# Kernel optimization log

Hardware: AMD Instinct MI355X
Metric: run time of the kernel (lower is better)

The kernel has to match this reference:

```python
import jax, jax.numpy as jnp
import numpy as np

B, S, D = 2, 2048, 2048
H, KVH, HD = 16, 4, 128
GROUPS = H // KVH
SCALE = HD ** -0.5


def rotate_half(x):
    half = x.shape[-1] // 2
    return jnp.concatenate((-x[..., half:], x[..., :half]), axis=-1)


def apply_rope(q, k, cos, sin):
    # q,k: [B,S,H,HD]; cos,sin: [S,HD//2] -> repeat_interleave(2) -> [S,HD]
    cos = jnp.repeat(cos, 2, axis=-1)[None, :, None, :]
    sin = jnp.repeat(sin, 2, axis=-1)[None, :, None, :]
    return q * cos + rotate_half(q) * sin, k * cos + rotate_half(k) * sin


def setup_inputs() -> dict:
    key = jax.random.key(0)
    ks = jax.random.split(key, 8)
    inp = {
        'x': jax.random.normal(ks[0], (B, S, D), dtype=jnp.float32),
        'cos': jnp.cos(jnp.arange(S, dtype=jnp.float32)[:, None] * (1.0 / (10000.0 ** (jnp.arange(HD // 2, dtype=jnp.float32) / (HD // 2))))[None, :].reshape(1, HD // 2)),
        'sin': None,
        'mask': jnp.tril(jnp.ones((S, S), dtype=bool))[None, None, :, :],
        'Wq': jax.random.normal(ks[1], (D, H * HD), dtype=jnp.float32) * (D ** -0.5),
        'Wk': jax.random.normal(ks[2], (D, KVH * HD), dtype=jnp.float32) * (D ** -0.5),
        'Wv': jax.random.normal(ks[3], (D, KVH * HD), dtype=jnp.float32) * (D ** -0.5),
        'Wo': jax.random.normal(ks[4], (H * HD, D), dtype=jnp.float32) * ((H * HD) ** -0.5),
    }
    inv_freq = 1.0 / (10000.0 ** (jnp.arange(0, HD // 2, dtype=jnp.float32) / (HD // 2)))
    freqs = jnp.arange(S, dtype=jnp.float32)[:, None] * inv_freq[None, :]  # [S, HD//2]
    inp['cos'] = jnp.cos(freqs)
    inp['sin'] = jnp.sin(freqs)
    return inp


def reference(x, cos, sin, mask, Wq, Wk, Wv, Wo):
    b, s, _ = x.shape
    q = (x @ Wq).reshape(b, s, H, HD)    # [B,S,H,HD]
    k = (x @ Wk).reshape(b, s, KVH, HD)  # [B,S,KVH,HD]
    v = (x @ Wv).reshape(b, s, KVH, HD)
    q, k = apply_rope(q, k, cos, sin)
    q = q.transpose(0, 2, 1, 3)  # [B,H,S,HD]
    k = k.transpose(0, 2, 1, 3)  # [B,KVH,S,HD]
    v = v.transpose(0, 2, 1, 3)
    k = jnp.repeat(k, GROUPS, axis=1)  # [B,H,S,HD]
    v = jnp.repeat(v, GROUPS, axis=1)
    scores = jnp.einsum('bhqd,bhkd->bhqk', q, k) * SCALE
    scores = jnp.where(mask, scores, -jnp.inf)
    attn = jax.nn.softmax(scores, axis=-1)
    out = jnp.einsum('bhqk,bhkd->bhqd', attn, v)
    out = out.transpose(0, 2, 1, 3).reshape(b, s, H * HD)
    return out @ Wo
```

## Files before the change

### kernel.cpp

```cpp
#include <hip/hip_runtime.h>
#include <hip/hip_bf16.h>
#include <cstdint>
#include <type_traits>

typedef __attribute__((ext_vector_type(8))) short short8;
typedef __attribute__((ext_vector_type(4))) float floatx4;

constexpr int S_LEN = 2048;
constexpr float ATTN_SCALE = 0.08838834764831845f;
constexpr float LOG2E = 1.4426950408889634f;
constexpr float CP = ATTN_SCALE * LOG2E;

__device__ __forceinline__ void gl_lds16(const void* gp, void* lp) {
  __builtin_amdgcn_global_load_lds(
      (__attribute__((address_space(1))) void*)(uintptr_t)gp,
      (__attribute__((address_space(3))) void*)lp,
      16, 0, 0);
}

__device__ __forceinline__ float rowmax16(float x) {
  union { float f; int i; } a, b;
  a.f = x;
  b.i = __builtin_amdgcn_update_dpp(0, a.i, 0x121, 0xF, 0xF, true);
  x = fmaxf(x, b.f); a.f = x;
  b.i = __builtin_amdgcn_update_dpp(0, a.i, 0x122, 0xF, 0xF, true);
  x = fmaxf(x, b.f); a.f = x;
  b.i = __builtin_amdgcn_update_dpp(0, a.i, 0x124, 0xF, 0xF, true);
  x = fmaxf(x, b.f); a.f = x;
  b.i = __builtin_amdgcn_update_dpp(0, a.i, 0x128, 0xF, 0xF, true);
  return fmaxf(x, b.f);
}

__device__ __forceinline__ void rope8(short8 x0, short8 x1, const float* ca,
                                      const float* sa, const float* cb,
                                      const float* sb, short8& y0, short8& y1) {
#pragma unroll
  for (int e = 0; e < 8; ++e) {
    union { short s; __hip_bfloat16 h; } u0, u1, w0, w1;
    u0.s = x0[e]; u1.s = x1[e];
    float f0 = __bfloat162float(u0.h), f1 = __bfloat162float(u1.h);
    int j = e >> 1;
    w0.h = __float2bfloat16(f0 * ca[j] - f1 * sa[j]);
    w1.h = __float2bfloat16(f1 * cb[j] + f0 * sb[j]);
    y0[e] = w0.s; y1[e] = w1.s;
  }
}

__device__ __forceinline__ void tr32(const float* __restrict__ src,
                                     __hip_bfloat16* __restrict__ dst,
                                     int blk, int nblk_x, int N, int tid,
                                     float (*tile)[33]) {
  int n0 = (blk % nblk_x) * 32, k0 = (blk / nblk_x) * 32;
  int tx = tid & 31, ty = tid >> 5;
#pragma unroll
  for (int i = ty; i < 32; i += 8)
    tile[i][tx] = src[(size_t)(k0 + i) * N + n0 + tx];
  __syncthreads();
#pragma unroll
  for (int i = ty; i < 32; i += 8)
    dst[(size_t)(n0 + i) * 2048 + k0 + tx] = __float2bfloat16(tile[tx][i]);
}

__global__ void prep_kernel(const float* __restrict__ x,
                            const float* __restrict__ Wq,
                            const float* __restrict__ Wk,
                            const float* __restrict__ Wv,
                            const float* __restrict__ Wo,
                            __hip_bfloat16* __restrict__ xb,
                            __hip_bfloat16* __restrict__ wqkvt,
                            __hip_bfloat16* __restrict__ wot) {
  __shared__ float tile[32][33];
  int bx = blockIdx.x, tid = threadIdx.x;
  if (bx < 8192) {
    int i = bx * 256 + tid;
    float4 f = reinterpret_cast<const float4*>(x)[i];
    union { unsigned long long u64; __hip_bfloat16 h[4]; } u;
    u.h[0] = __float2bfloat16(f.x);
    u.h[1] = __float2bfloat16(f.y);
    u.h[2] = __float2bfloat16(f.z);
    u.h[3] = __float2bfloat16(f.w);
    reinterpret_cast<unsigned long long*>(xb)[i] = u.u64;
  } else if (bx < 12288) {
    tr32(Wq, wqkvt, bx - 8192, 64, 2048, tid, tile);
  } else if (bx < 13312) {
    tr32(Wk, wqkvt + 2048 * 2048, bx - 12288, 16, 512, tid, tile);
  } else if (bx < 14336) {
    tr32(Wv, wqkvt + 2560 * 2048, bx - 13312, 16, 512, tid, tile);
  } else {
    tr32(Wo, wot, bx - 14336, 64, 2048, tid, tile);
  }
}

__global__ __launch_bounds__(256, 2) void qkv_gemm_kernel(
    const __hip_bfloat16* __restrict__ A,
    const __hip_bfloat16* __restrict__ Bt,
    __hip_bfloat16* __restrict__ qbuf,
    __hip_bfloat16* __restrict__ kbuf,
    __hip_bfloat16* __restrict__ vbuf,
    const float* __restrict__ cosb,
    const float* __restrict__ sinb) {
  constexpr int K = 2048;
  __shared__ __align__(16) __hip_bfloat16 lds[2 * 128 * 64];
  const int tid = threadIdx.x;
  const int wave = tid >> 6, lane = tid & 63;
  const int quad = lane >> 4, l15 = lane & 15;
  const int wm = wave >> 1, wn = wave & 1;
  const int m0 = blockIdx.y * 128, n0 = blockIdx.x * 128;

  floatx4 acc[4][4] = {};
  const __hip_bfloat16* Ab = A + (size_t)m0 * K;
  const __hip_bfloat16* Bb = Bt + (size_t)n0 * K;
  const int i0 = wave * 4;

  for (int k0 = 0; k0 < K; k0 += 64) {
#pragma unroll
    for (int j = 0; j < 4; ++j) {
      const int i = i0 + j;
      const int kchunk = i >> 1;
      const int row = ((i & 1) << 6) | lane;
      gl_lds16(Ab + (size_t)row * K + (k0 + kchunk * 8), &lds[i * 512]);
      gl_lds16(Bb + (size_t)row * K + (k0 + kchunk * 8), &lds[8192 + i * 512]);
    }
    __syncthreads();
#pragma unroll
    for (int kk = 0; kk < 2; ++kk) {
      short8 a[4], b[4];
#pragma unroll
      for (int mi = 0; mi < 4; ++mi)
        a[mi] = *(const short8*)&lds[((((kk << 2) | quad) * 128) + wm * 64 + mi * 16 + l15) * 8];
#pragma unroll
      for (int ni = 0; ni < 4; ++ni)
        b[ni] = *(const short8*)&lds[8192 + ((((kk << 2) | quad) * 128) + wn * 64 + ni * 16 + l15) * 8];
#pragma unroll
      for (int mi = 0; mi < 4; ++mi)
#pragma unroll
        for (int ni = 0; ni < 4; ++ni)
          acc[mi][ni] = __builtin_amdgcn_mfma_f32_16x16x32_bf16(a[mi], b[ni], acc[mi][ni], 0, 0, 0);
    }
    __syncthreads();
  }

  const bool isv = (n0 >= 2560);
  short* lds2 = (short*)lds;
#pragma unroll
  for (int mi = 0; mi < 4; ++mi)
#pragma unroll
    for (int ni = 0; ni < 4; ++ni)
#pragma unroll
      for (int r = 0; r < 4; ++r) {
        int row = wm * 64 + mi * 16 + quad * 4 + r;
        int col = wn * 64 + ni * 16 + l15;
        union { short s; __hip_bfloat16 h; } u;
        u.h = __float2bfloat16(acc[mi][ni][r]);
        if (isv) lds2[col * 128 + row] = u.s;
        else     lds2[row * 128 + col] = u.s;
      }
  __syncthreads();

  const int c8 = tid & 7, d0 = c8 * 8;
  if (n0 < 2048) {
#pragma unroll
    for (int j = 0; j < 4; ++j) {
      int rr = (tid >> 3) + 32 * j;
      int rowg = m0 + rr;
      int s = rowg & (S_LEN - 1);
      float ca[4], sa[4], cb[4], sb[4];
      *(float4*)ca = *(const float4*)&cosb[s * 64 + c8 * 4];
      *(float4*)sa = *(const float4*)&sinb[s * 64 + c8 * 4];
      *(float4*)cb = *(const float4*)&cosb[s * 64 + 32 + c8 * 4];
      *(float4*)sb = *(const float4*)&sinb[s * 64 + 32 + c8 * 4];
      short8 x0 = *(const short8*)&lds2[rr * 128 + d0];
      short8 x1 = *(const short8*)&lds2[rr * 128 + 64 + d0];
      short8 y0, y1;
      rope8(x0, x1, ca, sa, cb, sb, y0, y1);
      *(short8*)(qbuf + (size_t)rowg * 2048 + n0 + d0) = y0;
      *(short8*)(qbuf + (size_t)rowg * 2048 + n0 + 64 + d0) = y1;
    }
  } else if (!isv) {
    const int kvh = (n0 - 2048) >> 7;
#pragma unroll
    for (int j = 0; j < 4; ++j) {
      int rr = (tid >> 3) + 32 * j;
      int rowg = m0 + rr;
      int s = rowg & (S_LEN - 1), bb = rowg >> 11;
      int kv = s & 63;
      size_t tb = ((size_t)(bb * 4 + kvh) * 32 + (s >> 6)) * 8192;
      float ca[4], sa[4], cb[4], sb[4];
      *(float4*)ca = *(const float4*)&cosb[s * 64 + c8 * 4];
      *(float4*)sa = *(const float4*)&sinb[s * 64 + c8 * 4];
      *(float4*)cb = *(const float4*)&cosb[s * 64 + 32 + c8 * 4];
      *(float4*)sb = *(const float4*)&sinb[s * 64 + 32 + c8 * 4];
      short8 x0 = *(const short8*)&lds2[rr * 128 + d0];
      short8 x1 = *(const short8*)&lds2[rr * 128 + 64 + d0];
      short8 y0, y1;
      rope8(x0, x1, ca, sa, cb, sb, y0, y1);
      *(short8*)(kbuf + tb + (size_t)c8 * 512 + kv * 8) = y0;
      *(short8*)(kbuf + tb + (size_t)(8 + c8) * 512 + kv * 8) = y1;
    }
  } else {
    const int kvh = (n0 - 2560) >> 7;
    const int bb = m0 >> 11;
    const int kt0 = (m0 & (S_LEN - 1)) >> 6;
    const int kv0 = c8 * 8;
#pragma unroll
    for (int j = 0; j < 4; ++j) {
      int d = (tid >> 3) + 32 * j;
      int cxor = (d & 7) << 3;
#pragma unroll
      for (int half = 0; half < 2; ++half) {
        short8 vv = *(const short8*)&lds2[d * 128 + half * 64 + kv0];
        size_t tb = ((size_t)(bb * 4 + kvh) * 32 + kt0 + half) * 8192;
        *(short8*)(vbuf + tb + d * 64 + (kv0 ^ cxor)) = vv;
      }
    }
  }
}

__global__ __launch_bounds__(256, 2) void gemm_bt_f32_kernel(
    const __hip_bfloat16* __restrict__ A,
    const __hip_bfloat16* __restrict__ Bt,
    float* __restrict__ C, int N, int K) {
  __shared__ __align__(16) __hip_bfloat16 lds[2 * 128 * 64];
  const int tid = threadIdx.x;
  const int wave = tid >> 6, lane = tid & 63;
  const int quad = lane >> 4, l15 = lane & 15;
  const int wm = wave >> 1, wn = wave & 1;
  const int m0 = blockIdx.y * 128, n0 = blockIdx.x * 128;

  floatx4 acc[4][4] = {};
  const __hip_bfloat16* Ab = A + (size_t)m0 * K;
  const __hip_bfloat16* Bb = Bt + (size_t)n0 * K;
  const int i0 = wave * 4;

  for (int k0 = 0; k0 < K; k0 += 64) {
#pragma unroll
    for (int j = 0; j < 4; ++j) {
      const int i = i0 + j;
      const int kchunk = i >> 1;
      const int row = ((i & 1) << 6) | lane;
      gl_lds16(Ab + (size_t)row * K + (k0 + kchunk * 8), &lds[i * 512]);
      gl_lds16(Bb + (size_t)row * K + (k0 + kchunk * 8), &lds[8192 + i * 512]);
    }
    __syncthreads();
#pragma unroll
    for (int kk = 0; kk < 2; ++kk) {
      short8 a[4], b[4];
#pragma unroll
      for (int mi = 0; mi < 4; ++mi)
        a[mi] = *(const short8*)&lds[((((kk << 2) | quad) * 128) + wm * 64 + mi * 16 + l15) * 8];
#pragma unroll
      for (int ni = 0; ni < 4; ++ni)
        b[ni] = *(const short8*)&lds[8192 + ((((kk << 2) | quad) * 128) + wn * 64 + ni * 16 + l15) * 8];
#pragma unroll
      for (int mi = 0; mi < 4; ++mi)
#pragma unroll
        for (int ni = 0; ni < 4; ++ni)
          acc[mi][ni] = __builtin_amdgcn_mfma_f32_16x16x32_bf16(a[mi], b[ni], acc[mi][ni], 0, 0, 0);
    }
    __syncthreads();
  }

#pragma unroll
  for (int mi = 0; mi < 4; ++mi)
#pragma unroll
    for (int ni = 0; ni < 4; ++ni)
#pragma unroll
      for (int r = 0; r < 4; ++r) {
        int row = m0 + wm * 64 + mi * 16 + quad * 4 + r;
        int col = n0 + wn * 64 + ni * 16 + l15;
        C[(size_t)row * N + col] = acc[mi][ni][r];
      }
}

__global__ __launch_bounds__(256, 2) void attn_kernel(
    const __hip_bfloat16* __restrict__ qbuf,
    const __hip_bfloat16* __restrict__ kbuf,
    const __hip_bfloat16* __restrict__ vbuf,
    __hip_bfloat16* __restrict__ aout) {
  const int qt = (blockIdx.y & 16) ? blockIdx.x : (15 - blockIdx.x);
  const int bh = blockIdx.y;
  const int b = bh >> 4, h = bh & 15;
  const int kvh = h >> 2;

  __shared__ __align__(16) __hip_bfloat16 Kbuf[2][8192];
  __shared__ __align__(16) __hip_bfloat16 Vbuf[2][8192];
  __shared__ __align__(16) __hip_bfloat16 Plds[4 * 16 * 72];

  const int tid = threadIdx.x;
  const int wave = tid >> 6, lane = tid & 63;
  const int quad = lane >> 4, l15 = lane & 15;

  short8 qfrag[2][4];
#pragma unroll
  for (int rs = 0; rs < 2; ++rs)
#pragma unroll
    for (int kc = 0; kc < 4; ++kc)
      qfrag[rs][kc] = *(const short8*)(qbuf +
          (size_t)(b * S_LEN + qt * 128 + rs * 64 + wave * 16 + l15) * 2048 +
          h * 128 + kc * 32 + quad * 8);

  const __hip_bfloat16* ktiles = kbuf + (size_t)(b * 4 + kvh) * 32 * 8192;
  const __hip_bfloat16* vtiles = vbuf + (size_t)(b * 4 + kvh) * 32 * 8192;
  const int nt = 2 * qt + 2;

#pragma unroll
  for (int j = 0; j < 4; ++j) {
    int c = tid + 256 * j;
    gl_lds16(ktiles + c * 8, &Kbuf[0][c * 8]);
    gl_lds16(vtiles + c * 8, &Vbuf[0][c * 8]);
  }

  float m_r[2][4];
  floatx4 o[2][8] = {};
  floatx4 o_l[2] = {};
#pragma unroll
  for (int rs = 0; rs < 2; ++rs)
#pragma unroll
    for (int r = 0; r < 4; ++r) m_r[rs][r] = -1e30f;

  short8 onesb;
#pragma unroll
  for (int e = 0; e < 8; ++e) onesb[e] = (short)0x3F80;

  __hip_bfloat16* pw = &Plds[wave * 16 * 72];

  for (int kt = 0; kt < nt; ++kt) {
    const int cur = kt & 1;
    __syncthreads();

    if (kt + 1 < nt) {
      const __hip_bfloat16* kb = ktiles + (size_t)(kt + 1) * 8192;
      const __hip_bfloat16* vb = vtiles + (size_t)(kt + 1) * 8192;
#pragma unroll
      for (int j = 0; j < 4; ++j) {
        int c = tid + 256 * j;
        gl_lds16(kb + c * 8, &Kbuf[1 - cur][c * 8]);
        gl_lds16(vb + c * 8, &Vbuf[1 - cur][c * 8]);
      }
    }

    floatx4 sc[2][4] = {};
#pragma unroll
    for (int ni = 0; ni < 4; ++ni)
#pragma unroll
      for (int kc = 0; kc < 4; ++kc) {
        short8 bf = *(const short8*)&Kbuf[cur][((kc * 4 + quad) * 64 + ni * 16 + l15) * 8];
        sc[0][ni] = __builtin_amdgcn_mfma_f32_16x16x32_bf16(qfrag[0][kc], bf, sc[0][ni], 0, 0, 0);
        sc[1][ni] = __builtin_amdgcn_mfma_f32_16x16x32_bf16(qfrag[1][kc], bf, sc[1][ni], 0, 0, 0);
      }

    short8 pa[2][2];
#pragma unroll
    for (int rs = 0; rs < 2; ++rs) {
      const int qt64 = 2 * qt + rs;
      if (kt >= qt64) {
        const int qrow = qt * 128 + rs * 64 + wave * 16 + quad * 4;
#pragma unroll
        for (int ni = 0; ni < 4; ++ni) {
          int kvcol = kt * 64 + ni * 16 + l15;
#pragma unroll
          for (int r = 0; r < 4; ++r)
            if (kvcol > qrow + r) sc[rs][ni][r] = -1e30f;
        }
      }

      float alpha[4];
#pragma unroll
      for (int r = 0; r < 4; ++r) {
        float v = fmaxf(fmaxf(sc[rs][0][r], sc[rs][1][r]),
                        fmaxf(sc[rs][2][r], sc[rs][3][r]));
        v = rowmax16(v);
        float mnew = fmaxf(m_r[rs][r], v);
        alpha[r] = exp2f((m_r[rs][r] - mnew) * CP);
        m_r[rs][r] = mnew;
        float mc = mnew * CP;
#pragma unroll
        for (int ni = 0; ni < 4; ++ni) {
          float p = exp2f(sc[rs][ni][r] * CP - mc);
          pw[(quad * 4 + r) * 72 + ni * 16 + l15] = __float2bfloat16(p);
        }
      }

#pragma unroll
      for (int kk2 = 0; kk2 < 2; ++kk2)
        pa[rs][kk2] = *(const short8*)&pw[l15 * 72 + kk2 * 32 + quad * 8];

#pragma unroll
      for (int nc = 0; nc < 8; ++nc)
#pragma unroll
        for (int r = 0; r < 4; ++r) o[rs][nc][r] *= alpha[r];
#pragma unroll
      for (int r = 0; r < 4; ++r) o_l[rs][r] *= alpha[r];
    }

#pragma unroll
    for (int kk2 = 0; kk2 < 2; ++kk2) {
#pragma unroll
      for (int nc = 0; nc < 8; ++nc) {
        int d = nc * 16 + l15;
        int swcol = (kk2 * 32 + quad * 8) ^ ((d & 7) << 3);
        short8 vv = *(const short8*)&Vbuf[cur][d * 64 + swcol];
        o[0][nc] = __builtin_amdgcn_mfma_f32_16x16x32_bf16(pa[0][kk2], vv, o[0][nc], 0, 0, 0);
        o[1][nc] = __builtin_amdgcn_mfma_f32_16x16x32_bf16(pa[1][kk2], vv, o[1][nc], 0, 0, 0);
      }
      o_l[0] = __builtin_amdgcn_mfma_f32_16x16x32_bf16(pa[0][kk2], onesb, o_l[0], 0, 0, 0);
      o_l[1] = __builtin_amdgcn_mfma_f32_16x16x32_bf16(pa[1][kk2], onesb, o_l[1], 0, 0, 0);
    }
  }

#pragma unroll
  for (int rs = 0; rs < 2; ++rs) {
    float inv[4];
#pragma unroll
    for (int r = 0; r < 4; ++r) inv[r] = 1.0f / o_l[rs][r];
    const size_t orow0 = (size_t)(b * S_LEN + qt * 128 + rs * 64 + wave * 16 + quad * 4);
#pragma unroll
    for (int nc = 0; nc < 8; ++nc)
#pragma unroll
      for (int r = 0; r < 4; ++r)
        aout[(orow0 + r) * 2048 + h * 128 + nc * 16 + l15] =
            __float2bfloat16(o[rs][nc][r] * inv[r]);
  }
}

extern "C" void kernel_launch(void* const* d_in, const int* in_sizes, int n_in,
                              void* d_out, int out_size, void* d_ws, size_t ws_size,
                              hipStream_t stream) {
  const float* x    = (const float*)d_in[0];
  const float* cosb = (const float*)d_in[1];
  const float* sinb = (const float*)d_in[2];
  const float* Wq = (const float*)d_in[4];
  const float* Wk = (const float*)d_in[5];
  const float* Wv = (const float*)d_in[6];
  const float* Wo = (const float*)d_in[7];
  float* out = (float*)d_out;

  char* ws = (char*)d_ws;
  __hip_bfloat16* xb    = (__hip_bfloat16*)(ws);
  __hip_bfloat16* wqkvt = (__hip_bfloat16*)(ws + (16u << 20));
  __hip_bfloat16* wot   = (__hip_bfloat16*)(ws + (28u << 20));
  __hip_bfloat16* qbuf  = (__hip_bfloat16*)(ws + (36u << 20));
  __hip_bfloat16* kbuf  = (__hip_bfloat16*)(ws + (52u << 20));
  __hip_bfloat16* vbuf  = (__hip_bfloat16*)(ws + (56u << 20));
  __hip_bfloat16* aout  = (__hip_bfloat16*)(ws + (60u << 20));

  prep_kernel<<<18432, 256, 0, stream>>>(x, Wq, Wk, Wv, Wo, xb, wqkvt, wot);
  qkv_gemm_kernel<<<dim3(24, 32), 256, 0, stream>>>(xb, wqkvt, qbuf, kbuf, vbuf, cosb, sinb);
  attn_kernel<<<dim3(16, 32), 256, 0, stream>>>(qbuf, kbuf, vbuf, aout);
  gemm_bt_f32_kernel<<<dim3(16, 32), 256, 0, stream>>>(aout, wot, out, 2048, 2048);
}
```

Baseline: 413.2 us.

## Use 256x256 tiles with double-buffered pipelined core for both GEMMs

Replaces the 128x128 single-buffered GEMM loops with a shared 256x256-tile core using 512 threads. The core double-buffers LDS, prefetches A one step and B two steps ahead, and issues MFMAs under raised priority with fine-grained barriers. Epilogues are adapted to handle two heads per block. Larger tiles raise arithmetic intensity and hide load latency, but shrink the grids to 192 and 128 blocks, below the CU count, and the 128 KB LDS limits occupancy.

```diff
diff --git a/kernel.cpp b/kernel.cpp
--- a/kernel.cpp
+++ b/kernel.cpp
@@ -91,7 +91,93 @@
   }
 }
 
-__global__ __launch_bounds__(256, 2) void qkv_gemm_kernel(
+__device__ __forceinline__ void gemm256_core(
+    const __hip_bfloat16* __restrict__ Ab,
+    const __hip_bfloat16* __restrict__ Bb,
+    const int K, __hip_bfloat16* lds, floatx4 (&acc)[8][4]) {
+  const int tid = threadIdx.x;
+  const int wave = tid >> 6, lane = tid & 63;
+  const int quad = lane >> 4, l15 = lane & 15;
+  const int wm = wave >> 2, wn = wave & 3;
+  const int nt = K >> 6;
+  const int u2 = wave * 2;
+
+  auto stA = [&](int tt, int h) {
+    __hip_bfloat16* dst = lds + (tt & 1) * 32768;
+    const int k0 = tt << 6;
+#pragma unroll
+    for (int j = 0; j < 2; ++j) {
+      const int kc = (u2 + j) >> 1, rb = (u2 + j) & 1;
+      gl_lds16(Ab + (size_t)(h * 128 + rb * 64 + lane) * K + k0 + kc * 8,
+               dst + (kc * 256 + h * 128 + rb * 64) * 8);
+    }
+  };
+  auto stB = [&](int tt, int h) {
+    __hip_bfloat16* dst = lds + (tt & 1) * 32768 + 16384;
+    const int k0 = tt << 6;
+#pragma unroll
+    for (int j = 0; j < 2; ++j) {
+      const int kc = (u2 + j) >> 1, rb = (u2 + j) & 1;
+      gl_lds16(Bb + (size_t)(h * 128 + rb * 64 + lane) * K + k0 + kc * 8,
+               dst + (kc * 256 + h * 128 + rb * 64) * 8);
+    }
+  };
+
+  stA(0, 0); stA(0, 1); stB(0, 0); stB(0, 1);
+  if (nt > 1) { stB(1, 0); stB(1, 1); }
+  asm volatile("s_waitcnt vmcnt(4)" ::: "memory");
+  __builtin_amdgcn_s_barrier();
+
+  const int abase = (quad * 256 + wm * 128 + l15) * 8;
+  const int bbase = (quad * 256 + wn * 64 + l15) * 8;
+
+#pragma unroll 2
+  for (int t = 0; t < nt; ++t) {
+    const __hip_bfloat16* Al = lds + (t & 1) * 32768;
+    const __hip_bfloat16* Bl = Al + 16384;
+    short8 b[2][4];
+#pragma unroll
+    for (int q = 0; q < 4; ++q) {
+      short8 a[2][2];
+#pragma unroll
+      for (int kk = 0; kk < 2; ++kk) {
+        if (q == 0) {
+#pragma unroll
+          for (int ni = 0; ni < 4; ++ni)
+            b[kk][ni] = *(const short8*)&Bl[kk * 8192 + bbase + ni * 128];
+        }
+#pragma unroll
+        for (int mi = 0; mi < 2; ++mi)
+          a[kk][mi] = *(const short8*)&Al[kk * 8192 + abase + (2 * q + mi) * 128];
+      }
+      if (q == 0)      { if (t + 1 < nt) stA(t + 1, 0); }
+      else if (q == 1) { if (t + 1 < nt) stA(t + 1, 1); }
+      else if (q == 2) { if (t + 2 < nt) stB(t + 2, 0); }
+      else             { if (t + 2 < nt) stB(t + 2, 1); }
+      __builtin_amdgcn_s_barrier();
+      asm volatile("s_waitcnt lgkmcnt(0)" ::: "memory");
+      __builtin_amdgcn_sched_barrier(0);
+      __builtin_amdgcn_s_setprio(1);
+#pragma unroll
+      for (int kk = 0; kk < 2; ++kk)
+#pragma unroll
+        for (int mi = 0; mi < 2; ++mi)
+#pragma unroll
+          for (int ni = 0; ni < 4; ++ni)
+            acc[2 * q + mi][ni] = __builtin_amdgcn_mfma_f32_16x16x32_bf16(
+                a[kk][mi], b[kk][ni], acc[2 * q + mi][ni], 0, 0, 0);
+      __builtin_amdgcn_s_setprio(0);
+      if (q == 3) {
+        if (t + 2 < nt) asm volatile("s_waitcnt vmcnt(4)" ::: "memory");
+        else            asm volatile("s_waitcnt vmcnt(0)" ::: "memory");
+      }
+      __builtin_amdgcn_s_barrier();
+    }
+  }
+  asm volatile("" ::: "memory");
+}
+
+__global__ __launch_bounds__(512, 2) void qkv_gemm_kernel(
     const __hip_bfloat16* __restrict__ A,
     const __hip_bfloat16* __restrict__ Bt,
     __hip_bfloat16* __restrict__ qbuf,
@@ -100,68 +186,39 @@
     const float* __restrict__ cosb,
     const float* __restrict__ sinb) {
   constexpr int K = 2048;
-  __shared__ __align__(16) __hip_bfloat16 lds[2 * 128 * 64];
+  __shared__ __align__(16) __hip_bfloat16 lds[65536];
   const int tid = threadIdx.x;
+  const int m0 = blockIdx.y * 256, n0 = blockIdx.x * 256;
+
+  floatx4 acc[8][4] = {};
+  gemm256_core(A + (size_t)m0 * K, Bt + (size_t)n0 * K, K, lds, acc);
+
   const int wave = tid >> 6, lane = tid & 63;
   const int quad = lane >> 4, l15 = lane & 15;
-  const int wm = wave >> 1, wn = wave & 1;
-  const int m0 = blockIdx.y * 128, n0 = blockIdx.x * 128;
-
-  floatx4 acc[4][4] = {};
-  const __hip_bfloat16* Ab = A + (size_t)m0 * K;
-  const __hip_bfloat16* Bb = Bt + (size_t)n0 * K;
-  const int i0 = wave * 4;
-
-  for (int k0 = 0; k0 < K; k0 += 64) {
-#pragma unroll
-    for (int j = 0; j < 4; ++j) {
-      const int i = i0 + j;
-      const int kchunk = i >> 1;
-      const int row = ((i & 1) << 6) | lane;
-      gl_lds16(Ab + (size_t)row * K + (k0 + kchunk * 8), &lds[i * 512]);
-      gl_lds16(Bb + (size_t)row * K + (k0 + kchunk * 8), &lds[8192 + i * 512]);
-    }
-    __syncthreads();
-#pragma unroll
-    for (int kk = 0; kk < 2; ++kk) {
-      short8 a[4], b[4];
-#pragma unroll
-      for (int mi = 0; mi < 4; ++mi)
-        a[mi] = *(const short8*)&lds[((((kk << 2) | quad) * 128) + wm * 64 + mi * 16 + l15) * 8];
-#pragma unroll
-      for (int ni = 0; ni < 4; ++ni)
-        b[ni] = *(const short8*)&lds[8192 + ((((kk << 2) | quad) * 128) + wn * 64 + ni * 16 + l15) * 8];
-#pragma unroll
-      for (int mi = 0; mi < 4; ++mi)
-#pragma unroll
-        for (int ni = 0; ni < 4; ++ni)
-          acc[mi][ni] = __builtin_amdgcn_mfma_f32_16x16x32_bf16(a[mi], b[ni], acc[mi][ni], 0, 0, 0);
-    }
-    __syncthreads();
-  }
-
+  const int wm = wave >> 2, wn = wave & 3;
   const bool isv = (n0 >= 2560);
   short* lds2 = (short*)lds;
 #pragma unroll
-  for (int mi = 0; mi < 4; ++mi)
+  for (int mi = 0; mi < 8; ++mi)
 #pragma unroll
     for (int ni = 0; ni < 4; ++ni)
 #pragma unroll
       for (int r = 0; r < 4; ++r) {
-        int row = wm * 64 + mi * 16 + quad * 4 + r;
+        int row = wm * 128 + mi * 16 + quad * 4 + r;
         int col = wn * 64 + ni * 16 + l15;
         union { short s; __hip_bfloat16 h; } u;
         u.h = __float2bfloat16(acc[mi][ni][r]);
-        if (isv) lds2[col * 128 + row] = u.s;
-        else     lds2[row * 128 + col] = u.s;
+        if (isv) lds2[col * 256 + row] = u.s;
+        else     lds2[row * 256 + col] = u.s;
       }
   __syncthreads();
 
-  const int c8 = tid & 7, d0 = c8 * 8;
+  const int c16 = tid & 15, hh = c16 >> 3, c8 = c16 & 7;
+  const int rid = tid >> 4, d0 = c8 * 8;
   if (n0 < 2048) {
 #pragma unroll
-    for (int j = 0; j < 4; ++j) {
-      int rr = (tid >> 3) + 32 * j;
+    for (int j = 0; j < 8; ++j) {
+      int rr = rid + 32 * j;
       int rowg = m0 + rr;
       int s = rowg & (S_LEN - 1);
       float ca[4], sa[4], cb[4], sb[4];
@@ -169,18 +226,18 @@
       *(float4*)sa = *(const float4*)&sinb[s * 64 + c8 * 4];
       *(float4*)cb = *(const float4*)&cosb[s * 64 + 32 + c8 * 4];
       *(float4*)sb = *(const float4*)&sinb[s * 64 + 32 + c8 * 4];
-      short8 x0 = *(const short8*)&lds2[rr * 128 + d0];
-      short8 x1 = *(const short8*)&lds2[rr * 128 + 64 + d0];
+      short8 x0 = *(const short8*)&lds2[rr * 256 + hh * 128 + d0];
+      short8 x1 = *(const short8*)&lds2[rr * 256 + hh * 128 + 64 + d0];
       short8 y0, y1;
       rope8(x0, x1, ca, sa, cb, sb, y0, y1);
-      *(short8*)(qbuf + (size_t)rowg * 2048 + n0 + d0) = y0;
-      *(short8*)(qbuf + (size_t)rowg * 2048 + n0 + 64 + d0) = y1;
+      *(short8*)(qbuf + (size_t)rowg * 2048 + n0 + hh * 128 + d0) = y0;
+      *(short8*)(qbuf + (size_t)rowg * 2048 + n0 + hh * 128 + 64 + d0) = y1;
     }
   } else if (!isv) {
-    const int kvh = (n0 - 2048) >> 7;
-#pragma unroll
-    for (int j = 0; j < 4; ++j) {
-      int rr = (tid >> 3) + 32 * j;
+    const int kvh = ((n0 - 2048) >> 7) + hh;
+#pragma unroll
+    for (int j = 0; j < 8; ++j) {
+      int rr = rid + 32 * j;
       int rowg = m0 + rr;
       int s = rowg & (S_LEN - 1), bb = rowg >> 11;
       int kv = s & 63;
@@ -190,25 +247,25 @@
       *(float4*)sa = *(const float4*)&sinb[s * 64 + c8 * 4];
       *(float4*)cb = *(const float4*)&cosb[s * 64 + 32 + c8 * 4];
       *(float4*)sb = *(const float4*)&sinb[s * 64 + 32 + c8 * 4];
-      short8 x0 = *(const short8*)&lds2[rr * 128 + d0];
-      short8 x1 = *(const short8*)&lds2[rr * 128 + 64 + d0];
+      short8 x0 = *(const short8*)&lds2[rr * 256 + hh * 128 + d0];
+      short8 x1 = *(const short8*)&lds2[rr * 256 + hh * 128 + 64 + d0];
       short8 y0, y1;
       rope8(x0, x1, ca, sa, cb, sb, y0, y1);
       *(short8*)(kbuf + tb + (size_t)c8 * 512 + kv * 8) = y0;
       *(short8*)(kbuf + tb + (size_t)(8 + c8) * 512 + kv * 8) = y1;
     }
   } else {
-    const int kvh = (n0 - 2560) >> 7;
+    const int kvh = ((n0 - 2560) >> 7) + hh;
     const int bb = m0 >> 11;
     const int kt0 = (m0 & (S_LEN - 1)) >> 6;
     const int kv0 = c8 * 8;
 #pragma unroll
     for (int j = 0; j < 4; ++j) {
-      int d = (tid >> 3) + 32 * j;
+      int d = rid + 32 * j;
       int cxor = (d & 7) << 3;
 #pragma unroll
-      for (int half = 0; half < 2; ++half) {
-        short8 vv = *(const short8*)&lds2[d * 128 + half * 64 + kv0];
+      for (int half = 0; half < 4; ++half) {
+        short8 vv = *(const short8*)&lds2[(hh * 128 + d) * 256 + half * 64 + kv0];
         size_t tb = ((size_t)(bb * 4 + kvh) * 32 + kt0 + half) * 8192;
         *(short8*)(vbuf + tb + d * 64 + (kv0 ^ cxor)) = vv;
       }
@@ -216,57 +273,27 @@
   }
 }
 
-__global__ __launch_bounds__(256, 2) void gemm_bt_f32_kernel(
+__global__ __launch_bounds__(512, 2) void gemm_bt_f32_kernel(
     const __hip_bfloat16* __restrict__ A,
     const __hip_bfloat16* __restrict__ Bt,
     float* __restrict__ C, int N, int K) {
-  __shared__ __align__(16) __hip_bfloat16 lds[2 * 128 * 64];
+  __shared__ __align__(16) __hip_bfloat16 lds[65536];
   const int tid = threadIdx.x;
+  const int m0 = blockIdx.y * 256, n0 = blockIdx.x * 256;
+
+  floatx4 acc[8][4] = {};
+  gemm256_core(A + (size_t)m0 * K, Bt + (size_t)n0 * K, K, lds, acc);
+
   const int wave = tid >> 6, lane = tid & 63;
   const int quad = lane >> 4, l15 = lane & 15;
-  const int wm = wave >> 1, wn = wave & 1;
-  const int m0 = blockIdx.y * 128, n0 = blockIdx.x * 128;
-
-  floatx4 acc[4][4] = {};
-  const __hip_bfloat16* Ab = A + (size_t)m0 * K;
-  const __hip_bfloat16* Bb = Bt + (size_t)n0 * K;
-  const int i0 = wave * 4;
-
-  for (int k0 = 0; k0 < K; k0 += 64) {
-#pragma unroll
-    for (int j = 0; j < 4; ++j) {
-      const int i = i0 + j;
-      const int kchunk = i >> 1;
-      const int row = ((i & 1) << 6) | lane;
-      gl_lds16(Ab + (size_t)row * K + (k0 + kchunk * 8), &lds[i * 512]);
-      gl_lds16(Bb + (size_t)row * K + (k0 + kchunk * 8), &lds[8192 + i * 512]);
-    }
-    __syncthreads();
-#pragma unroll
-    for (int kk = 0; kk < 2; ++kk) {
-      short8 a[4], b[4];
-#pragma unroll
-      for (int mi = 0; mi < 4; ++mi)
-        a[mi] = *(const short8*)&lds[((((kk << 2) | quad) * 128) + wm * 64 + mi * 16 + l15) * 8];
-#pragma unroll
-      for (int ni = 0; ni < 4; ++ni)
-        b[ni] = *(const short8*)&lds[8192 + ((((kk << 2) | quad) * 128) + wn * 64 + ni * 16 + l15) * 8];
-#pragma unroll
-      for (int mi = 0; mi < 4; ++mi)
-#pragma unroll
-        for (int ni = 0; ni < 4; ++ni)
-          acc[mi][ni] = __builtin_amdgcn_mfma_f32_16x16x32_bf16(a[mi], b[ni], acc[mi][ni], 0, 0, 0);
-    }
-    __syncthreads();
-  }
-
-#pragma unroll
-  for (int mi = 0; mi < 4; ++mi)
+  const int wm = wave >> 2, wn = wave & 3;
+#pragma unroll
+  for (int mi = 0; mi < 8; ++mi)
 #pragma unroll
     for (int ni = 0; ni < 4; ++ni)
 #pragma unroll
       for (int r = 0; r < 4; ++r) {
-        int row = m0 + wm * 64 + mi * 16 + quad * 4 + r;
+        int row = m0 + wm * 128 + mi * 16 + quad * 4 + r;
         int col = n0 + wn * 64 + ni * 16 + l15;
         C[(size_t)row * N + col] = acc[mi][ni][r];
       }
@@ -445,7 +472,7 @@
   __hip_bfloat16* aout  = (__hip_bfloat16*)(ws + (60u << 20));
 
   prep_kernel<<<18432, 256, 0, stream>>>(x, Wq, Wk, Wv, Wo, xb, wqkvt, wot);
-  qkv_gemm_kernel<<<dim3(24, 32), 256, 0, stream>>>(xb, wqkvt, qbuf, kbuf, vbuf, cosb, sinb);
+  qkv_gemm_kernel<<<dim3(12, 16), 512, 0, stream>>>(xb, wqkvt, qbuf, kbuf, vbuf, cosb, sinb);
   attn_kernel<<<dim3(16, 32), 256, 0, stream>>>(qbuf, kbuf, vbuf, aout);
-  gemm_bt_f32_kernel<<<dim3(16, 32), 256, 0, stream>>>(aout, wot, out, 2048, 2048);
-}
+  gemm_bt_f32_kernel<<<dim3(8, 16), 512, 0, stream>>>(aout, wot, out, 2048, 2048);
+}
```

Measured after the change: 378.7 us. 8.4% less time.
